# Optimization experiments

Hardware: AMD Instinct MI355X
Metric: run time of the kernel (lower is better)

Reference implementation:

```python
import jax, jax.numpy as jnp
import numpy as np


def _gru_step(h, x, Wih, Whh, bih, bhh):
    # PyTorch GRU gate order: reset, update, new
    H = h.shape[-1]
    gx = x @ Wih.T + bih            # [B, 3H]
    gh = h @ Whh.T + bhh            # [B, 3H]
    r = jax.nn.sigmoid(gx[:, :H] + gh[:, :H])
    z = jax.nn.sigmoid(gx[:, H:2 * H] + gh[:, H:2 * H])
    n = jnp.tanh(gx[:, 2 * H:] + r * gh[:, 2 * H:])
    return (1.0 - z) * n + z * h


def setup_inputs() -> dict:
    key = jax.random.key(0)
    ks = jax.random.split(key, 20)
    B, S, L = 32, 200, 50
    Vt, Vs = 50000, 30000
    De, Ds, H = 256, 256, 512
    s = 0.05
    f = jnp.float32
    return {
        "method_code": jax.random.randint(ks[0], (B, S), 0, Vt),
        "method_summary": jax.random.randint(ks[1], (B, L), 0, Vs),
        "use_teacher": 1,
        "enc_emb": jax.random.normal(ks[2], (Vt, De), f) * s,
        "enc_Wih": jax.random.normal(ks[3], (3 * H, De), f) * s,
        "enc_Whh": jax.random.normal(ks[4], (3 * H, H), f) * s,
        "enc_bih": jax.random.normal(ks[5], (3 * H,), f) * s,
        "enc_bhh": jax.random.normal(ks[6], (3 * H,), f) * s,
        "dec_emb": jax.random.normal(ks[7], (Vs, Ds), f) * s,
        "dec_Wih": jax.random.normal(ks[8], (3 * H, Ds), f) * s,
        "dec_Whh": jax.random.normal(ks[9], (3 * H, H), f) * s,
        "dec_bih": jax.random.normal(ks[10], (3 * H,), f) * s,
        "dec_bhh": jax.random.normal(ks[11], (3 * H,), f) * s,
        "W1": jax.random.normal(ks[12], (H, 2 * H), f) * s,
        "b1": jax.random.normal(ks[13], (H,), f) * s,
        "W2": jax.random.normal(ks[14], (Vs, H), f) * s,
        "b2": jax.random.normal(ks[15], (Vs,), f) * s,
    }


def reference(method_code, method_summary, use_teacher,
              enc_emb, enc_Wih, enc_Whh, enc_bih, enc_bhh,
              dec_emb, dec_Wih, dec_Whh, dec_bih, dec_bhh,
              W1, b1, W2, b2):
    B = method_code.shape[0]
    H = enc_Whh.shape[1]
    # ---- GRU encoder over code tokens (hidden=None -> zeros) ----
    x_emb = enc_emb[method_code]                       # [B, S, De]
    h0 = jnp.zeros((B, H), x_emb.dtype)

    def enc_step(h, x):
        h = _gru_step(h, x, enc_Wih, enc_Whh, enc_bih, enc_bhh)
        return h, h

    h_last, enc_seq = jax.lax.scan(enc_step, h0, jnp.swapaxes(x_emb, 0, 1))
    enc_out = jnp.swapaxes(enc_seq, 0, 1)              # [B, S, H]

    # ---- attentive GRU decoder, teacher forcing (use_teacher=True) ----
    tokens = method_summary[:, :-1].T                  # [L-1, B]

    def dec_step(h, tok):
        emb = dec_emb[tok]                             # [B, Ds]
        h = _gru_step(h, emb, dec_Wih, dec_Whh, dec_bih, dec_bhh)
        attn = jax.nn.softmax(jnp.einsum('bh,bsh->bs', h, enc_out), axis=-1)
        ctx = jnp.einsum('bs,bsh->bh', attn, enc_out)  # [B, H]
        c = jnp.concatenate([ctx, h], axis=-1)         # [B, 2H]
        out = jax.nn.relu(c @ W1.T + b1) @ W2.T + b2   # [B, Vs]
        return h, out

    _, outs = jax.lax.scan(dec_step, h_last, tokens)   # [L-1, B, Vs]
    return jnp.swapaxes(outs, 0, 1)                    # [B, L-1, Vs]
```

## Files before the change

kernel.cpp:

```cpp
#include <hip/hip_runtime.h>
#include <cmath>

#define WGS  256
#define NWGR 256
#define DOMS 8
#define JGN  32
#define HBDW 2560

typedef float    f32x4 __attribute__((ext_vector_type(4)));
typedef unsigned u32x4 __attribute__((ext_vector_type(4)));
typedef short    s16x8 __attribute__((ext_vector_type(8)));
typedef unsigned short u16x4 __attribute__((ext_vector_type(4)));

#define B_   32
#define S_   200
#define L_   50
#define H_   512
#define DE_  256
#define VS_  30000
#define TD_  49
#define G3_  1536

#define OFF_ENC_OUT ((size_t)(S_*B_*G3_) + (size_t)(TD_*B_*G3_))
#define SZ_ENC_OUT  ((size_t)B_*S_*H_)
#define OFF_HBUF    (OFF_ENC_OUT + SZ_ENC_OUT)
#define SZ_HBUF     ((size_t)DOMS*2*HBDW)
#define OFF_CMAT    (OFF_HBUF + SZ_HBUF)
#define SZ_CMAT     ((size_t)TD_*B_*2*H_)
#define OFF_OUT1    (OFF_CMAT + SZ_CMAT)
#define SZ_OUT1     ((size_t)TD_*B_*H_)
#define OFF_W2HI    ((size_t)0)
#define OFF_W2LO    ((size_t)(VS_*H_/2))
#define OFF_O1HI    (OFF_OUT1 + SZ_OUT1)
#define OFF_O1LO    (OFF_O1HI + (size_t)(TD_*B_*H_/2))

#define RSTR 548
#define KBLK 68

__device__ __forceinline__ u32x4 load_u4_cc(const unsigned* p) {
  u32x4 v;
  asm volatile("global_load_dwordx4 %0, %1, off sc0 sc1" : "=v"(v) : "v"(p) : "memory");
  return v;
}

__device__ __forceinline__ float dot4(f32x4 a, f32x4 b) {
  return a.x * b.x + a.y * b.y + a.z * b.z + a.w * b.w;
}

__device__ __forceinline__ unsigned short f2bf(float f) {
  unsigned u = __float_as_uint(f);
  return (unsigned short)((u + 0x7fffu + ((u >> 16) & 1u)) >> 16);
}
__device__ __forceinline__ float bf2f(unsigned short h) {
  return __uint_as_float(((unsigned)h) << 16);
}

__global__ __launch_bounds__(WGS)
void recurrence_kernel(const int* __restrict__ mc, const int* __restrict__ ms,
                       const float* __restrict__ enc_emb,
                       const float* __restrict__ eWih, const float* __restrict__ eBih,
                       const float* __restrict__ dec_emb,
                       const float* __restrict__ dWih, const float* __restrict__ dBih,
                       const float* __restrict__ eWhh, const float* __restrict__ eBhh,
                       const float* __restrict__ dWhh, const float* __restrict__ dBhh,
                       float* __restrict__ enc_out,
                       float* __restrict__ hbuf,
                       float* __restrict__ Cmat)
{
  __shared__ float hlds[4 * RSTR];
  __shared__ float xlds[4 * 256];
  __shared__ float red[768];
  __shared__ float red2[768];

  const int t   = threadIdx.x;
  const int w   = blockIdx.x;
  const int dom = w >> 5;
  const int jg  = w & (JGN - 1);
  const int kh  = t >> 4;
  const int j   = (jg << 4) + (t & 15);
  const int bt_ = t >> 4;
  const int b_g = (dom << 2) + bt_;
  const int xb  = t >> 6, xc = t & 63;
  const int xb_g = (dom << 2) + xb;

  float* hdom = hbuf + (size_t)dom * (2 * HBDW);

  int rr[3], kb[3];
  #pragma unroll
  for (int i = 0; i < 3; ++i) {
    int g = i * 1024 + (t << 2);
    int blk = g / 80;
    rr[i] = g - blk * 80;
    kb[i] = blk << 4;
  }

  f32x4 whh[3][8];
  auto load_whh = [&](const float* __restrict__ W) {
    #pragma unroll
    for (int g = 0; g < 3; ++g)
      #pragma unroll
      for (int c = 0; c < 8; ++c)
        whh[g][c] = *(const f32x4*)(W + (size_t)(g * H_ + j) * H_ + (kh << 5) + (c << 2));
  };
  f32x4 wih[3][4];
  auto load_wih = [&](const float* __restrict__ W) {
    #pragma unroll
    for (int g = 0; g < 3; ++g)
      #pragma unroll
      for (int c = 0; c < 4; ++c)
        wih[g][c] = *(const f32x4*)(W + (size_t)(g * H_ + j) * DE_ + (kh << 4) + (c << 2));
  };
  load_whh(eWhh);
  load_wih(eWih);

  float bhr = 0.f, bhz = 0.f, bhn = 0.f, bxr = 0.f, bxz = 0.f, bxn = 0.f;
  if (t < 64) {
    bhr = eBhh[j]; bhz = eBhh[H_ + j]; bhn = eBhh[2 * H_ + j];
    bxr = eBih[j]; bxz = eBih[H_ + j]; bxn = eBih[2 * H_ + j];
  }

  for (int s = 0; s < S_ + TD_; ++s) {
    const bool enc = (s < S_);
    __syncthreads();
    if (s == S_) {
      load_whh(dWhh);
      load_wih(dWih);
      if (t < 64) {
        bhr = dBhh[j]; bhz = dBhh[H_ + j]; bhn = dBhh[2 * H_ + j];
        bxr = dBih[j]; bxz = dBih[H_ + j]; bxn = dBih[2 * H_ + j];
      }
    }

    {
      int tok = enc ? mc[xb_g * S_ + s] : ms[xb_g * L_ + (s - S_)];
      const float* emb = enc ? enc_emb : dec_emb;
      f32x4 xv = *(const f32x4*)(emb + (size_t)tok * DE_ + (xc << 2));
      *(f32x4*)&xlds[xb * 256 + (xc << 2)] = xv;
    }

    {
      const unsigned* hb = (const unsigned*)(hdom + (size_t)(s & 1) * HBDW);
      const unsigned tagreq = (unsigned)s;
      u32x4 v0, v1, v2;
      while (true) {
        v0 = load_u4_cc(hb + 0 * 1024 + (t << 2));
        v1 = load_u4_cc(hb + 1 * 1024 + (t << 2));
        if (t < 128) v2 = load_u4_cc(hb + 2 * 1024 + (t << 2));
        asm volatile("s_waitcnt vmcnt(0)" ::: "memory");
        bool ok = true;
        if ((rr[0] & 15) == 0) ok &= ((unsigned)v0.x >= tagreq);
        if ((rr[1] & 15) == 0) ok &= ((unsigned)v1.x >= tagreq);
        if (t < 128 && (rr[2] & 15) == 0) ok &= ((unsigned)v2.x >= tagreq);
        if (__all(ok)) break;
        __builtin_amdgcn_s_sleep(1);
      }
      #define SCAT(vv, ii) { \
        _Pragma("unroll") \
        for (int d = 0; d < 4; ++d) { \
          int pos = rr[ii] + d; \
          if ((pos & 15) != 0) { \
            int p = pos - 1 - (pos >> 4); \
            if (p < 64) { \
              int bb = p >> 4, k = kb[ii] + (p & 15); \
              hlds[bb * RSTR + ((k >> 6) * KBLK) + (k & 63)] = __uint_as_float(vv[d]); \
            } } } }
      SCAT(v0, 0) SCAT(v1, 1)
      if (t < 128) { SCAT(v2, 2) }
      #undef SCAT
    }
    __syncthreads();

    float acc[3][4], acx[3][4];
    #pragma unroll
    for (int g = 0; g < 3; ++g)
      #pragma unroll
      for (int b = 0; b < 4; ++b) { acc[g][b] = 0.f; acx[g][b] = 0.f; }

    const int hoff = (kh >> 1) * KBLK + (kh & 1) * 32;
    #pragma unroll
    for (int b = 0; b < 4; ++b) {
      const float* hp = &hlds[b * RSTR + hoff];
      #pragma unroll
      for (int c = 0; c < 8; ++c) {
        f32x4 hv = *(const f32x4*)(hp + (c << 2));
        acc[0][b] += dot4(whh[0][c], hv);
        acc[1][b] += dot4(whh[1][c], hv);
        acc[2][b] += dot4(whh[2][c], hv);
      }
      const float* xp = &xlds[b * 256 + (kh << 4)];
      #pragma unroll
      for (int c = 0; c < 4; ++c) {
        f32x4 xv = *(const f32x4*)(xp + (c << 2));
        acx[0][b] += dot4(wih[0][c], xv);
        acx[1][b] += dot4(wih[1][c], xv);
        acx[2][b] += dot4(wih[2][c], xv);
      }
    }

    #pragma unroll
    for (int g = 0; g < 3; ++g)
      #pragma unroll
      for (int b = 0; b < 4; ++b) {
        float v = acc[g][b];
        v += __shfl_xor(v, 16); v += __shfl_xor(v, 32);
        acc[g][b] = v;
        float u = acx[g][b];
        u += __shfl_xor(u, 16); u += __shfl_xor(u, 32);
        acx[g][b] = u;
      }
    if ((t & 48) == 0) {
      const int base = (t >> 6) * 192 + (t & 15) * 12;
      #pragma unroll
      for (int g = 0; g < 3; ++g)
        #pragma unroll
        for (int b = 0; b < 4; ++b) {
          red[base + g * 4 + b]  = acc[g][b];
          red2[base + g * 4 + b] = acx[g][b];
        }
    }
    __syncthreads();

    if (t < 64) {
      float ar = 0.f, az = 0.f, an = 0.f, xr = 0.f, xz = 0.f, xn = 0.f;
      #pragma unroll
      for (int ww = 0; ww < 4; ++ww) {
        const int base = ww * 192 + (t & 15) * 12 + bt_;
        ar += red[base];      az += red[base + 4];  an += red[base + 8];
        xr += red2[base];     xz += red2[base + 4]; xn += red2[base + 8];
      }
      float gxr = xr + bxr, gxz = xz + bxz, gxn = xn + bxn;
      float rg = 1.f / (1.f + expf(-(gxr + ar + bhr)));
      float zg = 1.f / (1.f + expf(-(gxz + az + bhz)));
      float ng = tanhf(gxn + rg * (an + bhn));
      float hprev = hlds[bt_ * RSTR + ((j >> 6) * KBLK) + (j & 63)];
      float hn = (1.f - zg) * ng + zg * hprev;
      if (enc) enc_out[((size_t)b_g * S_ + s) * H_ + j] = hn;
      else     Cmat[((size_t)(s - S_) * B_ + b_g) * (2 * H_) + H_ + j] = hn;

      unsigned* pb = (unsigned*)(hdom + (size_t)((s + 1) & 1) * HBDW) + jg * 80;
      const unsigned tagv = (unsigned)(s + 1);
      float vA = __shfl(hn, (t - 1 - (t >> 4)) & 63);
      unsigned valA = ((t & 15) == 0) ? tagv : __float_as_uint(vA);
      __hip_atomic_store(pb + t, valA, __ATOMIC_RELAXED, __HIP_MEMORY_SCOPE_AGENT);
      float vB = __shfl(hn, (59 + t) & 63);
      if (t < 16) {
        unsigned valB = (t == 0) ? tagv : __float_as_uint(vB);
        __hip_atomic_store(pb + 64 + t, valB, __ATOMIC_RELAXED, __HIP_MEMORY_SCOPE_AGENT);
      }
    }
  }
}

__global__ __launch_bounds__(WGS)
void attention_kernel(const float* __restrict__ enc_out,
                      float* __restrict__ Cmat)
{
  const int task = blockIdx.x;
  const int td = task >> 5, b = task & 31;
  const int t = threadIdx.x;
  const float* h = Cmat + ((size_t)td * B_ + b) * (2 * H_) + H_;

  __shared__ float red[WGS];
  __shared__ float p[WGS];

  float sv = -1e30f;
  if (t < S_) {
    const float* eo = enc_out + ((size_t)b * S_ + t) * H_;
    float acc = 0.f;
    #pragma unroll 4
    for (int k = 0; k < H_; k += 4) {
      float4 e = *(const float4*)(eo + k);
      float4 hv = *(const float4*)(h + k);
      acc += e.x * hv.x + e.y * hv.y + e.z * hv.z + e.w * hv.w;
    }
    sv = acc;
  }
  red[t] = sv; __syncthreads();
  for (int o = 128; o; o >>= 1) { if (t < o) red[t] = fmaxf(red[t], red[t + o]); __syncthreads(); }
  float mx = red[0]; __syncthreads();
  float ev = (t < S_) ? expf(sv - mx) : 0.f;
  red[t] = ev; __syncthreads();
  for (int o = 128; o; o >>= 1) { if (t < o) red[t] += red[t + o]; __syncthreads(); }
  float inv = 1.f / red[0];
  p[t] = ev * inv;
  __syncthreads();

  const float* eo = enc_out + (size_t)b * S_ * H_ + (t << 1);
  float ax = 0.f, ay = 0.f;
  for (int i = 0; i < S_; ++i) {
    float pi = p[i];
    float2 v = *(const float2*)(eo + (size_t)i * H_);
    ax += pi * v.x; ay += pi * v.y;
  }
  float* cd = Cmat + ((size_t)td * B_ + b) * (2 * H_) + (t << 1);
  cd[0] = ax; cd[1] = ay;
}

__launch_bounds__(WGS)
__global__ void gemm128_fc1(const float* __restrict__ A,
                            const float* __restrict__ Bw,
                            const float* __restrict__ bias,
                            unsigned short* __restrict__ Ohi,
                            unsigned short* __restrict__ Olo,
                            int M, int N, int K)
{
  const int APAD = 132;
  __shared__ float As[16 * APAD];
  __shared__ float Bs[16 * APAD];
  const int n0 = blockIdx.x * 128, m0 = blockIdx.y * 128;
  const int t = threadIdx.x;
  const int tx = t & 15, ty = t >> 4;

  float acc[8][8];
  #pragma unroll
  for (int i = 0; i < 8; ++i)
    #pragma unroll
    for (int jj = 0; jj < 8; ++jj) acc[i][jj] = 0.f;

  const int srow = t >> 2, skk = (t & 3) * 4;
  for (int k0 = 0; k0 < K; k0 += 16) {
    #pragma unroll
    for (int u = 0; u < 2; ++u) {
      int row = srow + u * 64;
      int m = m0 + row; if (m >= M) m = M - 1;
      f32x4 av = *(const f32x4*)(A + (size_t)m * K + k0 + skk);
      As[(skk + 0) * APAD + row] = av.x;
      As[(skk + 1) * APAD + row] = av.y;
      As[(skk + 2) * APAD + row] = av.z;
      As[(skk + 3) * APAD + row] = av.w;
      int n = n0 + row;
      f32x4 bv = *(const f32x4*)(Bw + (size_t)n * K + k0 + skk);
      Bs[(skk + 0) * APAD + row] = bv.x;
      Bs[(skk + 1) * APAD + row] = bv.y;
      Bs[(skk + 2) * APAD + row] = bv.z;
      Bs[(skk + 3) * APAD + row] = bv.w;
    }
    __syncthreads();
    #pragma unroll
    for (int k = 0; k < 16; ++k) {
      f32x4 a0 = *(const f32x4*)&As[k * APAD + ty * 8];
      f32x4 a1 = *(const f32x4*)&As[k * APAD + ty * 8 + 4];
      f32x4 b0 = *(const f32x4*)&Bs[k * APAD + tx * 4];
      f32x4 b1 = *(const f32x4*)&Bs[k * APAD + 64 + tx * 4];
      float a[8] = {a0.x, a0.y, a0.z, a0.w, a1.x, a1.y, a1.z, a1.w};
      float bb[8] = {b0.x, b0.y, b0.z, b0.w, b1.x, b1.y, b1.z, b1.w};
      #pragma unroll
      for (int i = 0; i < 8; ++i)
        #pragma unroll
        for (int jj = 0; jj < 8; ++jj)
          acc[i][jj] += a[i] * bb[jj];
    }
    __syncthreads();
  }

  #pragma unroll
  for (int i = 0; i < 8; ++i) {
    int m = m0 + ty * 8 + i;
    if (m >= M) continue;
    #pragma unroll
    for (int half = 0; half < 2; ++half) {
      u16x4 hv, lv;
      #pragma unroll
      for (int d = 0; d < 4; ++d) {
        int n = n0 + half * 64 + tx * 4 + d;
        float v = fmaxf(acc[i][half * 4 + d] + bias[n], 0.f);
        unsigned short hb = f2bf(v);
        hv[d] = hb;
        lv[d] = f2bf(v - bf2f(hb));
      }
      size_t o = (size_t)m * H_ + n0 + half * 64 + tx * 4;
      *(u16x4*)(Ohi + o) = hv;
      *(u16x4*)(Olo + o) = lv;
    }
  }
}

__global__ __launch_bounds__(WGS)
void cvt_split(const float* __restrict__ x, unsigned short* __restrict__ hi,
               unsigned short* __restrict__ lo, int n4)
{
  int i = blockIdx.x * WGS + threadIdx.x;
  if (i >= n4) return;
  f32x4 v = *(const f32x4*)(x + (size_t)i * 4);
  u16x4 h, l;
  #pragma unroll
  for (int d = 0; d < 4; ++d) {
    unsigned short hb = f2bf(v[d]);
    h[d] = hb;
    l[d] = f2bf(v[d] - bf2f(hb));
  }
  *(u16x4*)(hi + (size_t)i * 4) = h;
  *(u16x4*)(lo + (size_t)i * 4) = l;
}

__global__ __launch_bounds__(WGS)
void gemm_mfma_out(const unsigned short* __restrict__ Ahi,
                   const unsigned short* __restrict__ Alo,
                   const unsigned short* __restrict__ Bhi,
                   const unsigned short* __restrict__ Blo,
                   const float* __restrict__ bias,
                   float* __restrict__ out)
{
  __shared__ char smem[65536];
  const int t = threadIdx.x;
  const int l = t & 63;
  const int wv = t >> 6;
  const int r = l & 15, q = l >> 4;
  const int m0 = blockIdx.x * 128;
  const int n0 = blockIdx.y * 128;
  const int M = TD_ * B_, N = VS_, K = H_;
  const int wm = (wv >> 1) << 6;
  const int wn = (wv & 1) << 6;

  int swoff[2];
  size_t aoff[2], boff[2];
  #pragma unroll
  for (int qq = 0; qq < 2; ++qq) {
    int chunk = qq * 256 + t;
    int row = chunk >> 2, c = chunk & 3;
    swoff[qq] = row * 64 + ((c ^ ((row >> 1) & 3)) << 4);
    int gm = m0 + row; if (gm >= M) gm = M - 1;
    aoff[qq] = (size_t)gm * K + c * 8;
    int gn = n0 + row; if (gn >= N) gn = N - 1;
    boff[qq] = (size_t)gn * K + c * 8;
  }

  u32x4 rg[8];
  auto gload = [&](int k0) {
    #pragma unroll
    for (int qq = 0; qq < 2; ++qq) {
      rg[qq]     = *(const u32x4*)(Ahi + aoff[qq] + k0);
      rg[2 + qq] = *(const u32x4*)(Alo + aoff[qq] + k0);
      rg[4 + qq] = *(const u32x4*)(Bhi + boff[qq] + k0);
      rg[6 + qq] = *(const u32x4*)(Blo + boff[qq] + k0);
    }
  };
  auto swrite = [&](char* buf) {
    #pragma unroll
    for (int qq = 0; qq < 2; ++qq) {
      *(u32x4*)(buf +         swoff[qq]) = rg[qq];
      *(u32x4*)(buf +  8192 + swoff[qq]) = rg[2 + qq];
      *(u32x4*)(buf + 16384 + swoff[qq]) = rg[4 + qq];
      *(u32x4*)(buf + 24576 + swoff[qq]) = rg[6 + qq];
    }
  };

  int afo[4], bfo[4];
  #pragma unroll
  for (int fi = 0; fi < 4; ++fi) {
    int ra = wm + fi * 16 + r;
    afo[fi] = ra * 64 + ((q ^ ((ra >> 1) & 3)) << 4);
    int rb = wn + fi * 16 + r;
    bfo[fi] = rb * 64 + ((q ^ ((rb >> 1) & 3)) << 4);
  }

  f32x4 acc[4][4];
  #pragma unroll
  for (int fi = 0; fi < 4; ++fi)
    #pragma unroll
    for (int nj = 0; nj < 4; ++nj) acc[fi][nj] = (f32x4){0.f, 0.f, 0.f, 0.f};

  gload(0);
  swrite(smem);
  __syncthreads();
  int cur = 0;
  const int NS = K / 32;
  for (int s = 0; s < NS; ++s) {
    if (s + 1 < NS) gload((s + 1) * 32);
    char* buf = smem + cur * 32768;
    s16x8 ah[4], al[4], bh[4], bl[4];
    #pragma unroll
    for (int fi = 0; fi < 4; ++fi) {
      ah[fi] = *(const s16x8*)(buf +         afo[fi]);
      al[fi] = *(const s16x8*)(buf +  8192 + afo[fi]);
      bh[fi] = *(const s16x8*)(buf + 16384 + bfo[fi]);
      bl[fi] = *(const s16x8*)(buf + 24576 + bfo[fi]);
    }
    #pragma unroll
    for (int fi = 0; fi < 4; ++fi)
      #pragma unroll
      for (int nj = 0; nj < 4; ++nj) {
        acc[fi][nj] = __builtin_amdgcn_mfma_f32_16x16x32_bf16(ah[fi], bh[nj], acc[fi][nj], 0, 0, 0);
        acc[fi][nj] = __builtin_amdgcn_mfma_f32_16x16x32_bf16(ah[fi], bl[nj], acc[fi][nj], 0, 0, 0);
        acc[fi][nj] = __builtin_amdgcn_mfma_f32_16x16x32_bf16(al[fi], bh[nj], acc[fi][nj], 0, 0, 0);
      }
    if (s + 1 < NS) swrite(smem + (cur ^ 1) * 32768);
    __syncthreads();
    cur ^= 1;
  }

  #pragma unroll
  for (int nj = 0; nj < 4; ++nj) {
    int n = n0 + wn + nj * 16 + r;
    if (n >= N) continue;
    float bv = bias[n];
    #pragma unroll
    for (int fi = 0; fi < 4; ++fi) {
      #pragma unroll
      for (int e = 0; e < 4; ++e) {
        int m = m0 + wm + fi * 16 + q * 4 + e;
        if (m < M) {
          int bidx = m & 31, td = m >> 5;
          out[((size_t)bidx * TD_ + td) * (size_t)N + n] = acc[fi][nj][e] + bv;
        }
      }
    }
  }
}

extern "C" void kernel_launch(void* const* d_in, const int* in_sizes, int n_in,
                              void* d_out, int out_size, void* d_ws, size_t ws_size,
                              hipStream_t stream) {
  const int*   method_code    = (const int*)d_in[0];
  const int*   method_summary = (const int*)d_in[1];
  const float* enc_emb = (const float*)d_in[3];
  const float* enc_Wih = (const float*)d_in[4];
  const float* enc_Whh = (const float*)d_in[5];
  const float* enc_bih = (const float*)d_in[6];
  const float* enc_bhh = (const float*)d_in[7];
  const float* dec_emb = (const float*)d_in[8];
  const float* dec_Wih = (const float*)d_in[9];
  const float* dec_Whh = (const float*)d_in[10];
  const float* dec_bih = (const float*)d_in[11];
  const float* dec_bhh = (const float*)d_in[12];
  const float* W1 = (const float*)d_in[13];
  const float* b1 = (const float*)d_in[14];
  const float* W2 = (const float*)d_in[15];
  const float* b2 = (const float*)d_in[16];

  float* ws      = (float*)d_ws;
  float* enc_out = ws + OFF_ENC_OUT;
  float* hbuf    = ws + OFF_HBUF;
  float* Cmat    = ws + OFF_CMAT;
  unsigned short* W2hi = (unsigned short*)(ws + OFF_W2HI);
  unsigned short* W2lo = (unsigned short*)(ws + OFF_W2LO);
  unsigned short* O1hi = (unsigned short*)(ws + OFF_O1HI);
  unsigned short* O1lo = (unsigned short*)(ws + OFF_O1LO);

  hipMemsetAsync(hbuf, 0, SZ_HBUF * sizeof(float), stream);

  dim3 blk(WGS);

  recurrence_kernel<<<NWGR, blk, 0, stream>>>(
      method_code, method_summary,
      enc_emb, enc_Wih, enc_bih,
      dec_emb, dec_Wih, dec_bih,
      enc_Whh, enc_bhh, dec_Whh, dec_bhh,
      enc_out, hbuf, Cmat);

  attention_kernel<<<TD_ * B_, blk, 0, stream>>>(enc_out, Cmat);

  cvt_split<<<(VS_ * H_ / 4 + WGS - 1) / WGS, blk, 0, stream>>>(
      W2, W2hi, W2lo, VS_ * H_ / 4);

  gemm128_fc1<<<dim3(H_ / 128, (TD_ * B_ + 127) / 128), blk, 0, stream>>>(
      Cmat, W1, b1, O1hi, O1lo, TD_ * B_, H_, 2 * H_);

  gemm_mfma_out<<<dim3((TD_ * B_ + 127) / 128, (VS_ + 127) / 128), blk, 0, stream>>>(
      O1hi, O1lo, W2hi, W2lo, b2, (float*)d_out);
}
```

Measured before the change: 1.497 ms.

## Overlap input projection with recurrence, batch attention, retile FC GEMMs

The recurrence kernel now stages the next step's embedding and computes its input-gate projection after publishing h, so that work overlaps the wait for other workgroups' hidden state. The attention kernel handles four decoder steps per block, reusing each enc_out read across them, and uses wave-shuffle softmax. The FC1 GEMM moves to 64x64 tiles for more blocks, and the output MFMA GEMM uses 256-row tiles with a single LDS buffer and launch_bounds(WGS,1). The bigger output tile cuts W2 reloads but gives up double buffering and lowers occupancy.

```diff
diff --git a/kernel.cpp b/kernel.cpp
--- a/kernel.cpp
+++ b/kernel.cpp
@@ -6,6 +6,7 @@
 #define DOMS 8
 #define JGN  32
 #define HBDW 2560
+#define TDG  4
 
 typedef float    f32x4 __attribute__((ext_vector_type(4)));
 typedef unsigned u32x4 __attribute__((ext_vector_type(4)));
@@ -119,24 +120,55 @@
     bxr = eBih[j]; bxz = eBih[H_ + j]; bxn = eBih[2 * H_ + j];
   }
 
+  auto stage_x = [&](int s) {
+    const bool enc = (s < S_);
+    int tok = enc ? mc[xb_g * S_ + s] : ms[xb_g * L_ + (s - S_)];
+    const float* emb = enc ? enc_emb : dec_emb;
+    f32x4 xv = *(const f32x4*)(emb + (size_t)tok * DE_ + (xc << 2));
+    *(f32x4*)&xlds[xb * 256 + (xc << 2)] = xv;
+  };
+
+  auto compute_acx = [&]() {
+    float acx[3][4];
+    #pragma unroll
+    for (int g = 0; g < 3; ++g)
+      #pragma unroll
+      for (int b = 0; b < 4; ++b) acx[g][b] = 0.f;
+    #pragma unroll
+    for (int b = 0; b < 4; ++b) {
+      const float* xp = &xlds[b * 256 + (kh << 4)];
+      #pragma unroll
+      for (int c = 0; c < 4; ++c) {
+        f32x4 xv = *(const f32x4*)(xp + (c << 2));
+        acx[0][b] += dot4(wih[0][c], xv);
+        acx[1][b] += dot4(wih[1][c], xv);
+        acx[2][b] += dot4(wih[2][c], xv);
+      }
+    }
+    #pragma unroll
+    for (int g = 0; g < 3; ++g)
+      #pragma unroll
+      for (int b = 0; b < 4; ++b) {
+        float u = acx[g][b];
+        u += __shfl_xor(u, 16); u += __shfl_xor(u, 32);
+        acx[g][b] = u;
+      }
+    if ((t & 48) == 0) {
+      const int base = (t >> 6) * 192 + (t & 15) * 12;
+      #pragma unroll
+      for (int g = 0; g < 3; ++g)
+        #pragma unroll
+        for (int b = 0; b < 4; ++b)
+          red2[base + g * 4 + b] = acx[g][b];
+    }
+  };
+
+  stage_x(0);
+  __syncthreads();
+  compute_acx();
+
   for (int s = 0; s < S_ + TD_; ++s) {
     const bool enc = (s < S_);
-    __syncthreads();
-    if (s == S_) {
-      load_whh(dWhh);
-      load_wih(dWih);
-      if (t < 64) {
-        bhr = dBhh[j]; bhz = dBhh[H_ + j]; bhn = dBhh[2 * H_ + j];
-        bxr = dBih[j]; bxz = dBih[H_ + j]; bxn = dBih[2 * H_ + j];
-      }
-    }
-
-    {
-      int tok = enc ? mc[xb_g * S_ + s] : ms[xb_g * L_ + (s - S_)];
-      const float* emb = enc ? enc_emb : dec_emb;
-      f32x4 xv = *(const f32x4*)(emb + (size_t)tok * DE_ + (xc << 2));
-      *(f32x4*)&xlds[xb * 256 + (xc << 2)] = xv;
-    }
 
     {
       const unsigned* hb = (const unsigned*)(hdom + (size_t)(s & 1) * HBDW);
@@ -170,55 +202,44 @@
     }
     __syncthreads();
 
-    float acc[3][4], acx[3][4];
-    #pragma unroll
-    for (int g = 0; g < 3; ++g)
-      #pragma unroll
-      for (int b = 0; b < 4; ++b) { acc[g][b] = 0.f; acx[g][b] = 0.f; }
-
-    const int hoff = (kh >> 1) * KBLK + (kh & 1) * 32;
-    #pragma unroll
-    for (int b = 0; b < 4; ++b) {
-      const float* hp = &hlds[b * RSTR + hoff];
-      #pragma unroll
-      for (int c = 0; c < 8; ++c) {
-        f32x4 hv = *(const f32x4*)(hp + (c << 2));
-        acc[0][b] += dot4(whh[0][c], hv);
-        acc[1][b] += dot4(whh[1][c], hv);
-        acc[2][b] += dot4(whh[2][c], hv);
-      }
-      const float* xp = &xlds[b * 256 + (kh << 4)];
-      #pragma unroll
-      for (int c = 0; c < 4; ++c) {
-        f32x4 xv = *(const f32x4*)(xp + (c << 2));
-        acx[0][b] += dot4(wih[0][c], xv);
-        acx[1][b] += dot4(wih[1][c], xv);
-        acx[2][b] += dot4(wih[2][c], xv);
-      }
-    }
-
-    #pragma unroll
-    for (int g = 0; g < 3; ++g)
+    {
+      float acc[3][4];
+      #pragma unroll
+      for (int g = 0; g < 3; ++g)
+        #pragma unroll
+        for (int b = 0; b < 4; ++b) acc[g][b] = 0.f;
+      const int hoff = (kh >> 1) * KBLK + (kh & 1) * 32;
       #pragma unroll
       for (int b = 0; b < 4; ++b) {
-        float v = acc[g][b];
-        v += __shfl_xor(v, 16); v += __shfl_xor(v, 32);
-        acc[g][b] = v;
-        float u = acx[g][b];
-        u += __shfl_xor(u, 16); u += __shfl_xor(u, 32);
-        acx[g][b] = u;
-      }
-    if ((t & 48) == 0) {
-      const int base = (t >> 6) * 192 + (t & 15) * 12;
+        const float* hp = &hlds[b * RSTR + hoff];
+        #pragma unroll
+        for (int c = 0; c < 8; ++c) {
+          f32x4 hv = *(const f32x4*)(hp + (c << 2));
+          acc[0][b] += dot4(whh[0][c], hv);
+          acc[1][b] += dot4(whh[1][c], hv);
+          acc[2][b] += dot4(whh[2][c], hv);
+        }
+      }
       #pragma unroll
       for (int g = 0; g < 3; ++g)
         #pragma unroll
         for (int b = 0; b < 4; ++b) {
-          red[base + g * 4 + b]  = acc[g][b];
-          red2[base + g * 4 + b] = acx[g][b];
+          float v = acc[g][b];
+          v += __shfl_xor(v, 16); v += __shfl_xor(v, 32);
+          acc[g][b] = v;
         }
+      if ((t & 48) == 0) {
+        const int base = (t >> 6) * 192 + (t & 15) * 12;
+        #pragma unroll
+        for (int g = 0; g < 3; ++g)
+          #pragma unroll
+          for (int b = 0; b < 4; ++b)
+            red[base + g * 4 + b] = acc[g][b];
+      }
     }
     __syncthreads();
+
+    if (s + 1 < S_ + TD_) stage_x(s + 1);
 
     if (t < 64) {
       float ar = 0.f, az = 0.f, an = 0.f, xr = 0.f, xz = 0.f, xn = 0.f;
@@ -248,6 +269,19 @@
         __hip_atomic_store(pb + 64 + t, valB, __ATOMIC_RELAXED, __HIP_MEMORY_SCOPE_AGENT);
       }
     }
+    __syncthreads();
+
+    if (s + 1 < S_ + TD_) {
+      if (s + 1 == S_) {
+        load_whh(dWhh);
+        load_wih(dWih);
+        if (t < 64) {
+          bhr = dBhh[j]; bhz = dBhh[H_ + j]; bhn = dBhh[2 * H_ + j];
+          bxr = dBih[j]; bxz = dBih[H_ + j]; bxn = dBih[2 * H_ + j];
+        }
+      }
+      compute_acx();
+    }
   }
 }
 
@@ -255,123 +289,129 @@
 void attention_kernel(const float* __restrict__ enc_out,
                       float* __restrict__ Cmat)
 {
-  const int task = blockIdx.x;
-  const int td = task >> 5, b = task & 31;
+  const int blk = blockIdx.x;
+  const int b = blk / 13, ch = blk % 13;
   const int t = threadIdx.x;
-  const float* h = Cmat + ((size_t)td * B_ + b) * (2 * H_) + H_;
-
-  __shared__ float red[WGS];
-  __shared__ float p[WGS];
-
-  float sv = -1e30f;
+  __shared__ float hlds[TDG][512];
+  __shared__ float p[TDG][256];
+
+  for (int idx = t; idx < TDG * 128; idx += WGS) {
+    int u = idx >> 7, kq = (idx & 127) << 2;
+    int td = ch * TDG + u; if (td >= TD_) td = TD_ - 1;
+    *(f32x4*)&hlds[u][kq] =
+        *(const f32x4*)(Cmat + ((size_t)td * B_ + b) * (2 * H_) + H_ + kq);
+  }
+  __syncthreads();
+
+  float sv[TDG] = {0.f, 0.f, 0.f, 0.f};
   if (t < S_) {
     const float* eo = enc_out + ((size_t)b * S_ + t) * H_;
-    float acc = 0.f;
-    #pragma unroll 4
     for (int k = 0; k < H_; k += 4) {
-      float4 e = *(const float4*)(eo + k);
-      float4 hv = *(const float4*)(h + k);
-      acc += e.x * hv.x + e.y * hv.y + e.z * hv.z + e.w * hv.w;
-    }
-    sv = acc;
-  }
-  red[t] = sv; __syncthreads();
-  for (int o = 128; o; o >>= 1) { if (t < o) red[t] = fmaxf(red[t], red[t + o]); __syncthreads(); }
-  float mx = red[0]; __syncthreads();
-  float ev = (t < S_) ? expf(sv - mx) : 0.f;
-  red[t] = ev; __syncthreads();
-  for (int o = 128; o; o >>= 1) { if (t < o) red[t] += red[t + o]; __syncthreads(); }
-  float inv = 1.f / red[0];
-  p[t] = ev * inv;
+      f32x4 e = *(const f32x4*)(eo + k);
+      #pragma unroll
+      for (int u = 0; u < TDG; ++u) {
+        f32x4 hv = *(const f32x4*)&hlds[u][k];
+        sv[u] += e.x * hv.x + e.y * hv.y + e.z * hv.z + e.w * hv.w;
+      }
+    }
+  }
+  #pragma unroll
+  for (int u = 0; u < TDG; ++u) p[u][t] = (t < S_) ? sv[u] : -1e30f;
   __syncthreads();
 
+  {
+    const int wv = t >> 6, l = t & 63;
+    float m = fmaxf(fmaxf(p[wv][l], p[wv][l + 64]),
+                    fmaxf(p[wv][l + 128], p[wv][l + 192]));
+    for (int o = 32; o; o >>= 1) m = fmaxf(m, __shfl_xor(m, o));
+    float e0 = expf(p[wv][l] - m),       e1 = expf(p[wv][l + 64] - m);
+    float e2 = expf(p[wv][l + 128] - m), e3 = expf(p[wv][l + 192] - m);
+    float ssum = (e0 + e1) + (e2 + e3);
+    for (int o = 32; o; o >>= 1) ssum += __shfl_xor(ssum, o);
+    float inv = 1.f / ssum;
+    p[wv][l] = e0 * inv; p[wv][l + 64] = e1 * inv;
+    p[wv][l + 128] = e2 * inv; p[wv][l + 192] = e3 * inv;
+  }
+  __syncthreads();
+
+  float ax[TDG] = {0.f, 0.f, 0.f, 0.f}, ay[TDG] = {0.f, 0.f, 0.f, 0.f};
   const float* eo = enc_out + (size_t)b * S_ * H_ + (t << 1);
-  float ax = 0.f, ay = 0.f;
   for (int i = 0; i < S_; ++i) {
-    float pi = p[i];
     float2 v = *(const float2*)(eo + (size_t)i * H_);
-    ax += pi * v.x; ay += pi * v.y;
-  }
-  float* cd = Cmat + ((size_t)td * B_ + b) * (2 * H_) + (t << 1);
-  cd[0] = ax; cd[1] = ay;
+    #pragma unroll
+    for (int u = 0; u < TDG; ++u) {
+      float pi = p[u][i];
+      ax[u] += pi * v.x; ay[u] += pi * v.y;
+    }
+  }
+  #pragma unroll
+  for (int u = 0; u < TDG; ++u) {
+    int td = ch * TDG + u;
+    if (td < TD_) {
+      float* cd = Cmat + ((size_t)td * B_ + b) * (2 * H_) + (t << 1);
+      cd[0] = ax[u]; cd[1] = ay[u];
+    }
+  }
 }
 
 __launch_bounds__(WGS)
-__global__ void gemm128_fc1(const float* __restrict__ A,
-                            const float* __restrict__ Bw,
-                            const float* __restrict__ bias,
-                            unsigned short* __restrict__ Ohi,
-                            unsigned short* __restrict__ Olo,
-                            int M, int N, int K)
+__global__ void gemm64_fc1(const float* __restrict__ A,
+                           const float* __restrict__ Bw,
+                           const float* __restrict__ bias,
+                           unsigned short* __restrict__ Ohi,
+                           unsigned short* __restrict__ Olo)
 {
-  const int APAD = 132;
-  __shared__ float As[16 * APAD];
-  __shared__ float Bs[16 * APAD];
-  const int n0 = blockIdx.x * 128, m0 = blockIdx.y * 128;
+  const int M = TD_ * B_, N = H_, K = 2 * H_;
+  const int BK = 16;
+  __shared__ float As[BK][64];
+  __shared__ float Bs[BK][64];
+  const int m0 = blockIdx.y * 64, n0 = blockIdx.x * 64;
   const int t = threadIdx.x;
   const int tx = t & 15, ty = t >> 4;
-
-  float acc[8][8];
-  #pragma unroll
-  for (int i = 0; i < 8; ++i)
-    #pragma unroll
-    for (int jj = 0; jj < 8; ++jj) acc[i][jj] = 0.f;
-
-  const int srow = t >> 2, skk = (t & 3) * 4;
-  for (int k0 = 0; k0 < K; k0 += 16) {
-    #pragma unroll
-    for (int u = 0; u < 2; ++u) {
-      int row = srow + u * 64;
-      int m = m0 + row; if (m >= M) m = M - 1;
-      f32x4 av = *(const f32x4*)(A + (size_t)m * K + k0 + skk);
-      As[(skk + 0) * APAD + row] = av.x;
-      As[(skk + 1) * APAD + row] = av.y;
-      As[(skk + 2) * APAD + row] = av.z;
-      As[(skk + 3) * APAD + row] = av.w;
+  float acc[4][4] = {{0.f}};
+
+  const int row = t >> 2, kk = (t & 3) * 4;
+  for (int k0 = 0; k0 < K; k0 += BK) {
+    {
+      int m = m0 + row;
+      f32x4 v = {0.f, 0.f, 0.f, 0.f};
+      if (m < M) v = *(const f32x4*)(A + (size_t)m * K + k0 + kk);
+      As[kk][row] = v.x; As[kk + 1][row] = v.y; As[kk + 2][row] = v.z; As[kk + 3][row] = v.w;
       int n = n0 + row;
-      f32x4 bv = *(const f32x4*)(Bw + (size_t)n * K + k0 + skk);
-      Bs[(skk + 0) * APAD + row] = bv.x;
-      Bs[(skk + 1) * APAD + row] = bv.y;
-      Bs[(skk + 2) * APAD + row] = bv.z;
-      Bs[(skk + 3) * APAD + row] = bv.w;
+      f32x4 wv = *(const f32x4*)(Bw + (size_t)n * K + k0 + kk);
+      Bs[kk][row] = wv.x; Bs[kk + 1][row] = wv.y; Bs[kk + 2][row] = wv.z; Bs[kk + 3][row] = wv.w;
     }
     __syncthreads();
     #pragma unroll
-    for (int k = 0; k < 16; ++k) {
-      f32x4 a0 = *(const f32x4*)&As[k * APAD + ty * 8];
-      f32x4 a1 = *(const f32x4*)&As[k * APAD + ty * 8 + 4];
-      f32x4 b0 = *(const f32x4*)&Bs[k * APAD + tx * 4];
-      f32x4 b1 = *(const f32x4*)&Bs[k * APAD + 64 + tx * 4];
-      float a[8] = {a0.x, a0.y, a0.z, a0.w, a1.x, a1.y, a1.z, a1.w};
-      float bb[8] = {b0.x, b0.y, b0.z, b0.w, b1.x, b1.y, b1.z, b1.w};
-      #pragma unroll
-      for (int i = 0; i < 8; ++i)
+    for (int k = 0; k < BK; ++k) {
+      float a[4], bq[4];
+      *(f32x4*)a  = *(const f32x4*)&As[k][ty * 4];
+      *(f32x4*)bq = *(const f32x4*)&Bs[k][tx * 4];
+      #pragma unroll
+      for (int i = 0; i < 4; ++i)
         #pragma unroll
-        for (int jj = 0; jj < 8; ++jj)
-          acc[i][jj] += a[i] * bb[jj];
+        for (int jj = 0; jj < 4; ++jj)
+          acc[i][jj] += a[i] * bq[jj];
     }
     __syncthreads();
   }
 
   #pragma unroll
-  for (int i = 0; i < 8; ++i) {
-    int m = m0 + ty * 8 + i;
+  for (int i = 0; i < 4; ++i) {
+    int m = m0 + ty * 4 + i;
     if (m >= M) continue;
-    #pragma unroll
-    for (int half = 0; half < 2; ++half) {
-      u16x4 hv, lv;
-      #pragma unroll
-      for (int d = 0; d < 4; ++d) {
-        int n = n0 + half * 64 + tx * 4 + d;
-        float v = fmaxf(acc[i][half * 4 + d] + bias[n], 0.f);
-        unsigned short hb = f2bf(v);
-        hv[d] = hb;
-        lv[d] = f2bf(v - bf2f(hb));
-      }
-      size_t o = (size_t)m * H_ + n0 + half * 64 + tx * 4;
-      *(u16x4*)(Ohi + o) = hv;
-      *(u16x4*)(Olo + o) = lv;
-    }
+    u16x4 hv, lv;
+    #pragma unroll
+    for (int jj = 0; jj < 4; ++jj) {
+      int n = n0 + tx * 4 + jj;
+      float v = fmaxf(acc[i][jj] + bias[n], 0.f);
+      unsigned short hb = f2bf(v);
+      hv[jj] = hb;
+      lv[jj] = f2bf(v - bf2f(hb));
+    }
+    size_t o = (size_t)m * H_ + n0 + tx * 4;
+    *(u16x4*)(Ohi + o) = hv;
+    *(u16x4*)(Olo + o) = lv;
   }
 }
 
@@ -393,7 +433,7 @@
   *(u16x4*)(lo + (size_t)i * 4) = l;
 }
 
-__global__ __launch_bounds__(WGS)
+__global__ __launch_bounds__(WGS, 1)
 void gemm_mfma_out(const unsigned short* __restrict__ Ahi,
                    const unsigned short* __restrict__ Alo,
                    const unsigned short* __restrict__ Bhi,
@@ -401,92 +441,100 @@
                    const float* __restrict__ bias,
                    float* __restrict__ out)
 {
-  __shared__ char smem[65536];
+  __shared__ char smem[49152];
   const int t = threadIdx.x;
-  const int l = t & 63;
-  const int wv = t >> 6;
+  const int l = t & 63, wv = t >> 6;
   const int r = l & 15, q = l >> 4;
-  const int m0 = blockIdx.x * 128;
+  const int m0 = blockIdx.x * 256;
   const int n0 = blockIdx.y * 128;
   const int M = TD_ * B_, N = VS_, K = H_;
-  const int wm = (wv >> 1) << 6;
-  const int wn = (wv & 1) << 6;
-
-  int swoff[2];
-  size_t aoff[2], boff[2];
-  #pragma unroll
-  for (int qq = 0; qq < 2; ++qq) {
-    int chunk = qq * 256 + t;
-    int row = chunk >> 2, c = chunk & 3;
-    swoff[qq] = row * 64 + ((c ^ ((row >> 1) & 3)) << 4);
+  const int wm = (wv >> 1) * 128;
+  const int wn = (wv & 1) * 64;
+
+  int aswz[4]; size_t aoff[4];
+  #pragma unroll
+  for (int i = 0; i < 4; ++i) {
+    int ca = i * 256 + t;
+    int row = ca >> 2, cc = ca & 3;
+    aswz[i] = row * 64 + ((cc ^ ((row >> 1) & 3)) << 4);
     int gm = m0 + row; if (gm >= M) gm = M - 1;
-    aoff[qq] = (size_t)gm * K + c * 8;
+    aoff[i] = (size_t)gm * K + cc * 8;
+  }
+  int bswz[2]; size_t boff[2];
+  #pragma unroll
+  for (int i = 0; i < 2; ++i) {
+    int cb = i * 256 + t;
+    int row = cb >> 2, cc = cb & 3;
+    bswz[i] = row * 64 + ((cc ^ ((row >> 1) & 3)) << 4);
     int gn = n0 + row; if (gn >= N) gn = N - 1;
-    boff[qq] = (size_t)gn * K + c * 8;
-  }
-
-  u32x4 rg[8];
+    boff[i] = (size_t)gn * K + cc * 8;
+  }
+
+  u32x4 rg[12];
   auto gload = [&](int k0) {
     #pragma unroll
-    for (int qq = 0; qq < 2; ++qq) {
-      rg[qq]     = *(const u32x4*)(Ahi + aoff[qq] + k0);
-      rg[2 + qq] = *(const u32x4*)(Alo + aoff[qq] + k0);
-      rg[4 + qq] = *(const u32x4*)(Bhi + boff[qq] + k0);
-      rg[6 + qq] = *(const u32x4*)(Blo + boff[qq] + k0);
-    }
+    for (int i = 0; i < 4; ++i) rg[i]     = *(const u32x4*)(Ahi + aoff[i] + k0);
+    #pragma unroll
+    for (int i = 0; i < 4; ++i) rg[4 + i] = *(const u32x4*)(Alo + aoff[i] + k0);
+    #pragma unroll
+    for (int i = 0; i < 2; ++i) rg[8 + i] = *(const u32x4*)(Bhi + boff[i] + k0);
+    #pragma unroll
+    for (int i = 0; i < 2; ++i) rg[10 + i] = *(const u32x4*)(Blo + boff[i] + k0);
   };
-  auto swrite = [&](char* buf) {
-    #pragma unroll
-    for (int qq = 0; qq < 2; ++qq) {
-      *(u32x4*)(buf +         swoff[qq]) = rg[qq];
-      *(u32x4*)(buf +  8192 + swoff[qq]) = rg[2 + qq];
-      *(u32x4*)(buf + 16384 + swoff[qq]) = rg[4 + qq];
-      *(u32x4*)(buf + 24576 + swoff[qq]) = rg[6 + qq];
-    }
+  auto swrite = [&]() {
+    #pragma unroll
+    for (int i = 0; i < 4; ++i) *(u32x4*)(smem + aswz[i]) = rg[i];
+    #pragma unroll
+    for (int i = 0; i < 4; ++i) *(u32x4*)(smem + 16384 + aswz[i]) = rg[4 + i];
+    #pragma unroll
+    for (int i = 0; i < 2; ++i) *(u32x4*)(smem + 32768 + bswz[i]) = rg[8 + i];
+    #pragma unroll
+    for (int i = 0; i < 2; ++i) *(u32x4*)(smem + 40960 + bswz[i]) = rg[10 + i];
   };
 
-  int afo[4], bfo[4];
-  #pragma unroll
-  for (int fi = 0; fi < 4; ++fi) {
+  int afo[8], bfo[4];
+  #pragma unroll
+  for (int fi = 0; fi < 8; ++fi) {
     int ra = wm + fi * 16 + r;
     afo[fi] = ra * 64 + ((q ^ ((ra >> 1) & 3)) << 4);
-    int rb = wn + fi * 16 + r;
-    bfo[fi] = rb * 64 + ((q ^ ((rb >> 1) & 3)) << 4);
-  }
-
-  f32x4 acc[4][4];
-  #pragma unroll
-  for (int fi = 0; fi < 4; ++fi)
+  }
+  #pragma unroll
+  for (int nj = 0; nj < 4; ++nj) {
+    int rb = wn + nj * 16 + r;
+    bfo[nj] = rb * 64 + ((q ^ ((rb >> 1) & 3)) << 4);
+  }
+
+  f32x4 acc[8][4];
+  #pragma unroll
+  for (int fi = 0; fi < 8; ++fi)
     #pragma unroll
     for (int nj = 0; nj < 4; ++nj) acc[fi][nj] = (f32x4){0.f, 0.f, 0.f, 0.f};
 
   gload(0);
-  swrite(smem);
+  swrite();
   __syncthreads();
-  int cur = 0;
   const int NS = K / 32;
   for (int s = 0; s < NS; ++s) {
     if (s + 1 < NS) gload((s + 1) * 32);
-    char* buf = smem + cur * 32768;
-    s16x8 ah[4], al[4], bh[4], bl[4];
-    #pragma unroll
-    for (int fi = 0; fi < 4; ++fi) {
-      ah[fi] = *(const s16x8*)(buf +         afo[fi]);
-      al[fi] = *(const s16x8*)(buf +  8192 + afo[fi]);
-      bh[fi] = *(const s16x8*)(buf + 16384 + bfo[fi]);
-      bl[fi] = *(const s16x8*)(buf + 24576 + bfo[fi]);
-    }
-    #pragma unroll
-    for (int fi = 0; fi < 4; ++fi)
+    s16x8 bh[4], bl[4];
+    #pragma unroll
+    for (int nj = 0; nj < 4; ++nj) {
+      bh[nj] = *(const s16x8*)(smem + 32768 + bfo[nj]);
+      bl[nj] = *(const s16x8*)(smem + 40960 + bfo[nj]);
+    }
+    #pragma unroll
+    for (int fi = 0; fi < 8; ++fi) {
+      s16x8 ah = *(const s16x8*)(smem + afo[fi]);
+      s16x8 al = *(const s16x8*)(smem + 16384 + afo[fi]);
       #pragma unroll
       for (int nj = 0; nj < 4; ++nj) {
-        acc[fi][nj] = __builtin_amdgcn_mfma_f32_16x16x32_bf16(ah[fi], bh[nj], acc[fi][nj], 0, 0, 0);
-        acc[fi][nj] = __builtin_amdgcn_mfma_f32_16x16x32_bf16(ah[fi], bl[nj], acc[fi][nj], 0, 0, 0);
-        acc[fi][nj] = __builtin_amdgcn_mfma_f32_16x16x32_bf16(al[fi], bh[nj], acc[fi][nj], 0, 0, 0);
-      }
-    if (s + 1 < NS) swrite(smem + (cur ^ 1) * 32768);
+        acc[fi][nj] = __builtin_amdgcn_mfma_f32_16x16x32_bf16(ah, bh[nj], acc[fi][nj], 0, 0, 0);
+        acc[fi][nj] = __builtin_amdgcn_mfma_f32_16x16x32_bf16(ah, bl[nj], acc[fi][nj], 0, 0, 0);
+        acc[fi][nj] = __builtin_amdgcn_mfma_f32_16x16x32_bf16(al, bh[nj], acc[fi][nj], 0, 0, 0);
+      }
+    }
     __syncthreads();
-    cur ^= 1;
+    if (s + 1 < NS) { swrite(); __syncthreads(); }
   }
 
   #pragma unroll
@@ -495,7 +543,7 @@
     if (n >= N) continue;
     float bv = bias[n];
     #pragma unroll
-    for (int fi = 0; fi < 4; ++fi) {
+    for (int fi = 0; fi < 8; ++fi) {
       #pragma unroll
       for (int e = 0; e < 4; ++e) {
         int m = m0 + wm + fi * 16 + q * 4 + e;
@@ -548,14 +596,14 @@
       enc_Whh, enc_bhh, dec_Whh, dec_bhh,
       enc_out, hbuf, Cmat);
 
-  attention_kernel<<<TD_ * B_, blk, 0, stream>>>(enc_out, Cmat);
+  attention_kernel<<<B_ * 13, blk, 0, stream>>>(enc_out, Cmat);
 
   cvt_split<<<(VS_ * H_ / 4 + WGS - 1) / WGS, blk, 0, stream>>>(
       W2, W2hi, W2lo, VS_ * H_ / 4);
 
-  gemm128_fc1<<<dim3(H_ / 128, (TD_ * B_ + 127) / 128), blk, 0, stream>>>(
-      Cmat, W1, b1, O1hi, O1lo, TD_ * B_, H_, 2 * H_);
-
-  gemm_mfma_out<<<dim3((TD_ * B_ + 127) / 128, (VS_ + 127) / 128), blk, 0, stream>>>(
+  gemm64_fc1<<<dim3(H_ / 64, (TD_ * B_ + 63) / 64), blk, 0, stream>>>(
+      Cmat, W1, b1, O1hi, O1lo);
+
+  gemm_mfma_out<<<dim3((TD_ * B_ + 255) / 256, (VS_ + 127) / 128), blk, 0, stream>>>(
       O1hi, O1lo, W2hi, W2lo, b2, (float*)d_out);
 }
```

After: 1.407 ms. 6.0% less time.
